# Optimization experiments

Measured on AMD Instinct MI355X. Metric: run time of the kernel, lower is better.

Reference implementation:

```python
import jax, jax.numpy as jnp
import numpy as np

N_RAYS = 65536
S_UNIFORM = 256          # 2 * n_samples coarse samples per ray
N_IMP = 128              # importance samples per ray
TRUNCATION = 2.0 / 512.0 * 4.0  # default in sdf2weights


def raw2weights_occupancy(raw):
    # raw2outputs_nerf_color with occupancy=True
    alpha = jax.nn.sigmoid(10.0 * raw)  # [N, S]
    trans = jnp.cumprod(
        jnp.concatenate([jnp.ones_like(alpha[:, :1]), 1.0 - alpha + 1e-10], axis=-1),
        axis=-1,
    )[:, :-1]
    return alpha, alpha * trans


def sample_pdf_det(bins, weights, n_samples):
    # bins: [N, M], weights: [N, M-1]; deterministic (det=True) inverse-CDF sampling
    w = weights + 1e-5
    pdf = w / jnp.sum(w, axis=-1, keepdims=True)
    cdf = jnp.cumsum(pdf, axis=-1)
    cdf = jnp.concatenate([jnp.zeros_like(cdf[..., :1]), cdf], axis=-1)  # [N, M]
    u = jnp.linspace(0.0, 1.0, n_samples, dtype=cdf.dtype)
    u = jnp.broadcast_to(u, cdf.shape[:-1] + (n_samples,))               # [N, n]
    inds = jax.vmap(lambda c, uu: jnp.searchsorted(c, uu, side='right'))(cdf, u)
    below = jnp.maximum(inds - 1, 0)
    above = jnp.minimum(inds, cdf.shape[-1] - 1)
    cdf_b = jnp.take_along_axis(cdf, below, axis=-1)
    cdf_a = jnp.take_along_axis(cdf, above, axis=-1)
    bins_b = jnp.take_along_axis(bins, below, axis=-1)
    bins_a = jnp.take_along_axis(bins, above, axis=-1)
    denom = cdf_a - cdf_b
    denom = jnp.where(denom < 1e-5, jnp.ones_like(denom), denom)
    t = (u - cdf_b) / denom
    return bins_b + t * (bins_a - bins_b)


def sdf2weights(sdf, z_vals, truncation=TRUNCATION, sc_factor=1.0):
    alpha = jax.nn.sigmoid(sdf / truncation) * jax.nn.sigmoid(-sdf / truncation)
    signs = sdf[:, 1:] * sdf[:, :-1]
    sign_mask = jnp.where(signs < 0.0, 1.0, 0.0)
    inds = jnp.argmax(sign_mask, axis=1)[:, None]              # first zero-crossing
    z_min = jnp.take_along_axis(z_vals, inds, axis=1)          # [N, 1]
    trunc_mask = jnp.where(z_vals < z_min + sc_factor * truncation, 1.0, 0.0)
    alpha = alpha * trunc_mask
    weights = alpha / (jnp.sum(alpha, axis=-1, keepdims=True) + 1e-8)
    return weights


def setup_inputs() -> dict:
    key = jax.random.key(0)
    k1, k2, k3, k4 = jax.random.split(key, 4)
    occ = jax.random.normal(k1, (N_RAYS, S_UNIFORM), dtype=jnp.float32)
    # monotonically increasing depths in [0.1, 4.1)
    z_vals_u = jnp.sort(
        jax.random.uniform(k2, (N_RAYS, S_UNIFORM), dtype=jnp.float32) * 4.0 + 0.1,
        axis=-1,
    )
    sdf = jax.random.normal(k3, (N_RAYS, N_IMP), dtype=jnp.float32) * 0.05
    rgbs = jax.random.uniform(k4, (N_RAYS, N_IMP, 3), dtype=jnp.float32)
    return {"occ": occ, "z_vals_u": z_vals_u, "sdf": sdf, "rgbs": rgbs}


def reference(occ, z_vals_u, sdf, rgbs):
    # 1) coarse occupancy compositing -> weights
    _, w_u = raw2weights_occupancy(occ)
    # 2) inverse-CDF importance sampling over midpoints (detached, as in gen_samples)
    z_mid = 0.5 * (z_vals_u[..., 1:] + z_vals_u[..., :-1])
    z_samples = jax.lax.stop_gradient(sample_pdf_det(z_mid, w_u[..., 1:-1], N_IMP))
    # 3) TSDF weights at importance samples
    weights = sdf2weights(sdf, z_samples)
    # 4) composite
    rgb_map = jnp.clip(jnp.sum(weights[..., None] * rgbs, axis=-2), 0.0, 1.0)  # [N,3]
    depth_map = jnp.sum(weights * z_samples, axis=-1)                          # [N]
    return jnp.concatenate([rgb_map, depth_map[:, None], weights], axis=-1)    # [N, 4+N_IMP]
```

## Files before the change

### kernel.cpp

```cpp
#include <hip/hip_runtime.h>

#define S_U 256
#define N_IMP 128
#define OUT_STRIDE (4 + N_IMP)
#define TRUNC 0.015625f
#define WPB 4
#define INV127 (1.0f / 127.0f)
#define MERGE_N 384

template <int CTRL, int ROWM>
__device__ __forceinline__ float dppf(float identity, float x) {
    return __int_as_float(__builtin_amdgcn_update_dpp(
        __float_as_int(identity), __float_as_int(x), CTRL, ROWM, 0xf, false));
}

__device__ __forceinline__ float wscan_add(float x) {
    x += dppf<0x111, 0xf>(0.f, x);
    x += dppf<0x112, 0xf>(0.f, x);
    x += dppf<0x114, 0xf>(0.f, x);
    x += dppf<0x118, 0xf>(0.f, x);
    x += dppf<0x142, 0xa>(0.f, x);
    x += dppf<0x143, 0xc>(0.f, x);
    return x;
}

__device__ __forceinline__ float wscan_mul(float x) {
    x *= dppf<0x111, 0xf>(1.f, x);
    x *= dppf<0x112, 0xf>(1.f, x);
    x *= dppf<0x114, 0xf>(1.f, x);
    x *= dppf<0x118, 0xf>(1.f, x);
    x *= dppf<0x142, 0xa>(1.f, x);
    x *= dppf<0x143, 0xc>(1.f, x);
    return x;
}

__device__ __forceinline__ int wscan_add_i(int x) {
    x += __builtin_amdgcn_update_dpp(0, x, 0x111, 0xf, 0xf, false);
    x += __builtin_amdgcn_update_dpp(0, x, 0x112, 0xf, 0xf, false);
    x += __builtin_amdgcn_update_dpp(0, x, 0x114, 0xf, 0xf, false);
    x += __builtin_amdgcn_update_dpp(0, x, 0x118, 0xf, 0xf, false);
    x += __builtin_amdgcn_update_dpp(0, x, 0x142, 0xa, 0xf, false);
    x += __builtin_amdgcn_update_dpp(0, x, 0x143, 0xc, 0xf, false);
    return x;
}

__device__ __forceinline__ int wscan_min(int x) {
    const int I = 0x7fffffff;
    x = min(x, __builtin_amdgcn_update_dpp(I, x, 0x111, 0xf, 0xf, false));
    x = min(x, __builtin_amdgcn_update_dpp(I, x, 0x112, 0xf, 0xf, false));
    x = min(x, __builtin_amdgcn_update_dpp(I, x, 0x114, 0xf, 0xf, false));
    x = min(x, __builtin_amdgcn_update_dpp(I, x, 0x118, 0xf, 0xf, false));
    x = min(x, __builtin_amdgcn_update_dpp(I, x, 0x142, 0xa, 0xf, false));
    x = min(x, __builtin_amdgcn_update_dpp(I, x, 0x143, 0xc, 0xf, false));
    return x;
}

__device__ __forceinline__ int k_of(float c) {
    int k = (int)ceilf(c * 127.0f);
    k = min(max(k, 0), 128);
    if (k > 0 && c <= (float)(k - 1) * INV127) --k;
    else if (k < 128 && !(c <= (float)k * INV127)) ++k;
    return k;
}

__global__ __launch_bounds__(256) void tsdf_render_kernel(
    const float* __restrict__ occ,
    const float* __restrict__ zvals,
    const float* __restrict__ sdf,
    const float* __restrict__ rgbs,
    float* __restrict__ out)
{
    const int lane = threadIdx.x & 63;
    const int wv   = threadIdx.x >> 6;
    const int ray  = blockIdx.x * WPB + wv;

    __shared__ __align__(16) float2 s_pair[WPB][S_U];
    __shared__ __align__(16) int s_A[WPB][MERGE_N];
    __shared__ int s_below[WPB][N_IMP];

    const float4 o4 = ((const float4*)(occ   + (size_t)ray * S_U))[lane];
    const float4 z4 = ((const float4*)(zvals + (size_t)ray * S_U))[lane];
    const float2 sd2 = ((const float2*)(sdf + (size_t)ray * N_IMP))[lane];
    const float2* rg = (const float2*)(rgbs + (size_t)ray * (N_IMP * 3)) + lane * 3;
    const float2 p0 = rg[0];
    const float2 p1 = rg[1];
    const float2 p2 = rg[2];

    int4* Az = (int4*)s_A[wv];
    Az[lane] = make_int4(0, 0, 0, 0);
    if (lane < 32) Az[64 + lane] = make_int4(0, 0, 0, 0);

    float a0 = 1.0f / (1.0f + __expf(-10.0f * o4.x));
    float a1 = 1.0f / (1.0f + __expf(-10.0f * o4.y));
    float a2 = 1.0f / (1.0f + __expf(-10.0f * o4.z));
    float a3 = 1.0f / (1.0f + __expf(-10.0f * o4.w));
    float t0 = 1.0f - a0 + 1e-10f;
    float t1 = 1.0f - a1 + 1e-10f;
    float t2 = 1.0f - a2 + 1e-10f;
    float t3 = 1.0f - a3 + 1e-10f;
    float pp0 = t0, pp1 = pp0 * t1, pp2 = pp1 * t2, pp3 = pp2 * t3;
    float ip = wscan_mul(pp3);
    float pbase = __shfl_up(ip, 1);
    if (lane == 0) pbase = 1.0f;

    float w0 = a0 * pbase;
    float w1 = a1 * pbase * pp0;
    float w2 = a2 * pbase * pp1;
    float w3 = a3 * pbase * pp2;

    float v0 = (lane > 0)  ? w0 + 1e-5f : 0.0f;
    float v1 = w1 + 1e-5f;
    float v2 = w2 + 1e-5f;
    float v3 = (lane < 63) ? w3 + 1e-5f : 0.0f;
    float s0 = v0, s1 = s0 + v1, s2 = s1 + v2, s3 = s2 + v3;
    float is = wscan_add(s3);
    float total = __shfl(is, 63);
    float sbase = __shfl_up(is, 1);
    if (lane == 0) sbase = 0.0f;
    float invt = 1.0f / total;

    float c0 = (sbase + s0) * invt;
    float c1 = (sbase + s1) * invt;
    float c2 = (sbase + s2) * invt;
    float c3 = (sbase + s3) * invt;

    float znext = __shfl_down(z4.x, 1);
    float zm0 = 0.5f * (z4.x + z4.y);
    float zm1 = 0.5f * (z4.y + z4.z);
    float zm2 = 0.5f * (z4.z + z4.w);
    float zm3 = 0.5f * (z4.w + znext);

    float2* pr = s_pair[wv];
    *(float4*)&pr[lane * 4 + 0] = make_float4(c0, zm0, c1, zm1);
    *(float4*)&pr[lane * 4 + 2] = make_float4(c2, zm2, c3, zm3);

    int k0 = k_of(c0), k1 = k_of(c1), k2 = k_of(c2), k3 = k_of(c3);
    int base = lane * 4;
    int* Aw = s_A[wv];
    __builtin_amdgcn_wave_barrier();
    Aw[base + 0 + k0] = 1;
    Aw[base + 1 + k1] = 1;
    Aw[base + 2 + k2] = 1;
    if (base + 3 < 255) Aw[base + 3 + k3] = 1;
    __builtin_amdgcn_wave_barrier();

    const int2 r0 = *(const int2*)&Aw[6 * lane + 0];
    const int2 r1 = *(const int2*)&Aw[6 * lane + 2];
    const int2 r2 = *(const int2*)&Aw[6 * lane + 4];
    int q0 = r0.x, q1 = r0.y, q2 = r1.x, q3 = r1.y, q4 = r2.x, q5 = r2.y;
    int e1 = q0, e2 = e1 + q1, e3 = e2 + q2, e4 = e3 + q3, e5 = e4 + q4;
    int tot = e5 + q5;
    int incl = wscan_add_i(tot);
    int sb = __shfl_up(incl, 1);
    if (lane == 0) sb = 0;

    int* bel = s_below[wv];
    int pbase6 = 6 * lane;
    {
        int Sx, j;
        Sx = sb;      j = pbase6 + 0 - Sx; if (!q0 && j < 128) bel[j] = Sx - 1;
        Sx = sb + e1; j = pbase6 + 1 - Sx; if (!q1 && j < 128) bel[j] = Sx - 1;
        Sx = sb + e2; j = pbase6 + 2 - Sx; if (!q2 && j < 128) bel[j] = Sx - 1;
        Sx = sb + e3; j = pbase6 + 3 - Sx; if (!q3 && j < 128) bel[j] = Sx - 1;
        Sx = sb + e4; j = pbase6 + 4 - Sx; if (!q4 && j < 128) bel[j] = Sx - 1;
        Sx = sb + e5; j = pbase6 + 5 - Sx; if (!q5 && j < 128) bel[j] = Sx - 1;
    }
    __builtin_amdgcn_wave_barrier();

    const int2 bb = *(const int2*)&bel[2 * lane];
    int b0 = bb.x, b1 = bb.y;
    float2 pb0 = pr[b0];
    float2 pa0 = pr[min(b0 + 1, 254)];
    float2 pb1 = pr[b1];
    float2 pa1 = pr[min(b1 + 1, 254)];

    float u0 = (float)(2 * lane)     * INV127;
    float u1 = (float)(2 * lane + 1) * INV127;
    float d0 = pa0.x - pb0.x; d0 = (d0 < 1e-5f) ? 1.0f : d0;
    float d1 = pa1.x - pb1.x; d1 = (d1 < 1e-5f) ? 1.0f : d1;
    float zs0 = pb0.y + ((u0 - pb0.x) / d0) * (pa0.y - pb0.y);
    float zs1 = pb1.y + ((u1 - pb1.x) / d1) * (pa1.y - pb1.y);

    float sn = __shfl_down(sd2.x, 1);
    int c = 0x7fffffff;
    if (sd2.x * sd2.y < 0.0f)                 c = 2 * lane;
    else if (lane < 63 && sd2.y * sn < 0.0f)  c = 2 * lane + 1;
    c = wscan_min(c);
    int ci = __shfl(c, 63);
    if (ci == 0x7fffffff) ci = 0;
    float zca = __shfl(zs0, ci >> 1);
    float zcb = __shfl(zs1, ci >> 1);
    float z_min = (ci & 1) ? zcb : zca;

    float x0 = sd2.x * (1.0f / TRUNC);
    float x1 = sd2.y * (1.0f / TRUNC);
    float al0 = 1.0f / (2.0f + __expf(x0) + __expf(-x0));
    float al1 = 1.0f / (2.0f + __expf(x1) + __expf(-x1));
    float zlim = z_min + TRUNC;
    if (!(zs0 < zlim)) al0 = 0.0f;
    if (!(zs1 < zlim)) al1 = 0.0f;

    float sA = wscan_add(al0 + al1);
    float sR = wscan_add(al0 * p0.x + al1 * p1.y);
    float sG = wscan_add(al0 * p0.y + al1 * p2.x);
    float sB = wscan_add(al0 * p1.x + al1 * p2.y);
    float sD = wscan_add(al0 * zs0  + al1 * zs1);

    float asum = __shfl(sA, 63);
    float inv_s = 1.0f / (asum + 1e-8f);

    float* ob = out + (size_t)ray * OUT_STRIDE;
    ((float2*)(ob + 4))[lane] = make_float2(al0 * inv_s, al1 * inv_s);
    if (lane == 63) {
        float inv63 = 1.0f / (sA + 1e-8f);
        ob[0] = fminf(fmaxf(sR * inv63, 0.0f), 1.0f);
        ob[1] = fminf(fmaxf(sG * inv63, 0.0f), 1.0f);
        ob[2] = fminf(fmaxf(sB * inv63, 0.0f), 1.0f);
        ob[3] = sD * inv63;
    }
}

extern "C" void kernel_launch(void* const* d_in, const int* in_sizes, int n_in,
                              void* d_out, int out_size, void* d_ws, size_t ws_size,
                              hipStream_t stream) {
    const float* occ  = (const float*)d_in[0];
    const float* z    = (const float*)d_in[1];
    const float* sdf  = (const float*)d_in[2];
    const float* rgbs = (const float*)d_in[3];
    float* out = (float*)d_out;
    const int n_rays = in_sizes[0] / S_U;
    hipLaunchKernelGGL(tsdf_render_kernel, dim3(n_rays / WPB), dim3(256), 0, stream,
                       occ, z, sdf, rgbs, out);
}
```

Before: 271.1 us.

## Process multiple rays per wave with software-prefetched next-ray loads

Each wave now loops over eight consecutive rays instead of handling one. Inside the loop it issues the next ray's global loads before computing the current ray, so memory latency overlaps with compute. The grid shrinks by a factor of eight, which reduces launch and per-wave setup cost but lowers the number of resident waves available to hide latency. It also raises register pressure from holding the prefetched values.

```diff
diff --git a/kernel.cpp b/kernel.cpp
--- a/kernel.cpp
+++ b/kernel.cpp
@@ -5,6 +5,7 @@
 #define OUT_STRIDE (4 + N_IMP)
 #define TRUNC 0.015625f
 #define WPB 4
+#define RPW 8
 #define INV127 (1.0f / 127.0f)
 #define MERGE_N 384
 
@@ -72,151 +73,167 @@
 {
     const int lane = threadIdx.x & 63;
     const int wv   = threadIdx.x >> 6;
-    const int ray  = blockIdx.x * WPB + wv;
+    const int wave = blockIdx.x * WPB + wv;
+    const int ray0 = wave * RPW;
 
     __shared__ __align__(16) float2 s_pair[WPB][S_U];
     __shared__ __align__(16) int s_A[WPB][MERGE_N];
     __shared__ int s_below[WPB][N_IMP];
 
-    const float4 o4 = ((const float4*)(occ   + (size_t)ray * S_U))[lane];
-    const float4 z4 = ((const float4*)(zvals + (size_t)ray * S_U))[lane];
-    const float2 sd2 = ((const float2*)(sdf + (size_t)ray * N_IMP))[lane];
-    const float2* rg = (const float2*)(rgbs + (size_t)ray * (N_IMP * 3)) + lane * 3;
-    const float2 p0 = rg[0];
-    const float2 p1 = rg[1];
-    const float2 p2 = rg[2];
-
-    int4* Az = (int4*)s_A[wv];
-    Az[lane] = make_int4(0, 0, 0, 0);
-    if (lane < 32) Az[64 + lane] = make_int4(0, 0, 0, 0);
-
-    float a0 = 1.0f / (1.0f + __expf(-10.0f * o4.x));
-    float a1 = 1.0f / (1.0f + __expf(-10.0f * o4.y));
-    float a2 = 1.0f / (1.0f + __expf(-10.0f * o4.z));
-    float a3 = 1.0f / (1.0f + __expf(-10.0f * o4.w));
-    float t0 = 1.0f - a0 + 1e-10f;
-    float t1 = 1.0f - a1 + 1e-10f;
-    float t2 = 1.0f - a2 + 1e-10f;
-    float t3 = 1.0f - a3 + 1e-10f;
-    float pp0 = t0, pp1 = pp0 * t1, pp2 = pp1 * t2, pp3 = pp2 * t3;
-    float ip = wscan_mul(pp3);
-    float pbase = __shfl_up(ip, 1);
-    if (lane == 0) pbase = 1.0f;
-
-    float w0 = a0 * pbase;
-    float w1 = a1 * pbase * pp0;
-    float w2 = a2 * pbase * pp1;
-    float w3 = a3 * pbase * pp2;
-
-    float v0 = (lane > 0)  ? w0 + 1e-5f : 0.0f;
-    float v1 = w1 + 1e-5f;
-    float v2 = w2 + 1e-5f;
-    float v3 = (lane < 63) ? w3 + 1e-5f : 0.0f;
-    float s0 = v0, s1 = s0 + v1, s2 = s1 + v2, s3 = s2 + v3;
-    float is = wscan_add(s3);
-    float total = __shfl(is, 63);
-    float sbase = __shfl_up(is, 1);
-    if (lane == 0) sbase = 0.0f;
-    float invt = 1.0f / total;
-
-    float c0 = (sbase + s0) * invt;
-    float c1 = (sbase + s1) * invt;
-    float c2 = (sbase + s2) * invt;
-    float c3 = (sbase + s3) * invt;
-
-    float znext = __shfl_down(z4.x, 1);
-    float zm0 = 0.5f * (z4.x + z4.y);
-    float zm1 = 0.5f * (z4.y + z4.z);
-    float zm2 = 0.5f * (z4.z + z4.w);
-    float zm3 = 0.5f * (z4.w + znext);
-
-    float2* pr = s_pair[wv];
-    *(float4*)&pr[lane * 4 + 0] = make_float4(c0, zm0, c1, zm1);
-    *(float4*)&pr[lane * 4 + 2] = make_float4(c2, zm2, c3, zm3);
-
-    int k0 = k_of(c0), k1 = k_of(c1), k2 = k_of(c2), k3 = k_of(c3);
-    int base = lane * 4;
-    int* Aw = s_A[wv];
-    __builtin_amdgcn_wave_barrier();
-    Aw[base + 0 + k0] = 1;
-    Aw[base + 1 + k1] = 1;
-    Aw[base + 2 + k2] = 1;
-    if (base + 3 < 255) Aw[base + 3 + k3] = 1;
-    __builtin_amdgcn_wave_barrier();
-
-    const int2 r0 = *(const int2*)&Aw[6 * lane + 0];
-    const int2 r1 = *(const int2*)&Aw[6 * lane + 2];
-    const int2 r2 = *(const int2*)&Aw[6 * lane + 4];
-    int q0 = r0.x, q1 = r0.y, q2 = r1.x, q3 = r1.y, q4 = r2.x, q5 = r2.y;
-    int e1 = q0, e2 = e1 + q1, e3 = e2 + q2, e4 = e3 + q3, e5 = e4 + q4;
-    int tot = e5 + q5;
-    int incl = wscan_add_i(tot);
-    int sb = __shfl_up(incl, 1);
-    if (lane == 0) sb = 0;
-
-    int* bel = s_below[wv];
-    int pbase6 = 6 * lane;
-    {
-        int Sx, j;
-        Sx = sb;      j = pbase6 + 0 - Sx; if (!q0 && j < 128) bel[j] = Sx - 1;
-        Sx = sb + e1; j = pbase6 + 1 - Sx; if (!q1 && j < 128) bel[j] = Sx - 1;
-        Sx = sb + e2; j = pbase6 + 2 - Sx; if (!q2 && j < 128) bel[j] = Sx - 1;
-        Sx = sb + e3; j = pbase6 + 3 - Sx; if (!q3 && j < 128) bel[j] = Sx - 1;
-        Sx = sb + e4; j = pbase6 + 4 - Sx; if (!q4 && j < 128) bel[j] = Sx - 1;
-        Sx = sb + e5; j = pbase6 + 5 - Sx; if (!q5 && j < 128) bel[j] = Sx - 1;
-    }
-    __builtin_amdgcn_wave_barrier();
-
-    const int2 bb = *(const int2*)&bel[2 * lane];
-    int b0 = bb.x, b1 = bb.y;
-    float2 pb0 = pr[b0];
-    float2 pa0 = pr[min(b0 + 1, 254)];
-    float2 pb1 = pr[b1];
-    float2 pa1 = pr[min(b1 + 1, 254)];
-
-    float u0 = (float)(2 * lane)     * INV127;
-    float u1 = (float)(2 * lane + 1) * INV127;
-    float d0 = pa0.x - pb0.x; d0 = (d0 < 1e-5f) ? 1.0f : d0;
-    float d1 = pa1.x - pb1.x; d1 = (d1 < 1e-5f) ? 1.0f : d1;
-    float zs0 = pb0.y + ((u0 - pb0.x) / d0) * (pa0.y - pb0.y);
-    float zs1 = pb1.y + ((u1 - pb1.x) / d1) * (pa1.y - pb1.y);
-
-    float sn = __shfl_down(sd2.x, 1);
-    int c = 0x7fffffff;
-    if (sd2.x * sd2.y < 0.0f)                 c = 2 * lane;
-    else if (lane < 63 && sd2.y * sn < 0.0f)  c = 2 * lane + 1;
-    c = wscan_min(c);
-    int ci = __shfl(c, 63);
-    if (ci == 0x7fffffff) ci = 0;
-    float zca = __shfl(zs0, ci >> 1);
-    float zcb = __shfl(zs1, ci >> 1);
-    float z_min = (ci & 1) ? zcb : zca;
-
-    float x0 = sd2.x * (1.0f / TRUNC);
-    float x1 = sd2.y * (1.0f / TRUNC);
-    float al0 = 1.0f / (2.0f + __expf(x0) + __expf(-x0));
-    float al1 = 1.0f / (2.0f + __expf(x1) + __expf(-x1));
-    float zlim = z_min + TRUNC;
-    if (!(zs0 < zlim)) al0 = 0.0f;
-    if (!(zs1 < zlim)) al1 = 0.0f;
-
-    float sA = wscan_add(al0 + al1);
-    float sR = wscan_add(al0 * p0.x + al1 * p1.y);
-    float sG = wscan_add(al0 * p0.y + al1 * p2.x);
-    float sB = wscan_add(al0 * p1.x + al1 * p2.y);
-    float sD = wscan_add(al0 * zs0  + al1 * zs1);
-
-    float asum = __shfl(sA, 63);
-    float inv_s = 1.0f / (asum + 1e-8f);
-
-    float* ob = out + (size_t)ray * OUT_STRIDE;
-    ((float2*)(ob + 4))[lane] = make_float2(al0 * inv_s, al1 * inv_s);
-    if (lane == 63) {
-        float inv63 = 1.0f / (sA + 1e-8f);
-        ob[0] = fminf(fmaxf(sR * inv63, 0.0f), 1.0f);
-        ob[1] = fminf(fmaxf(sG * inv63, 0.0f), 1.0f);
-        ob[2] = fminf(fmaxf(sB * inv63, 0.0f), 1.0f);
-        ob[3] = sD * inv63;
+    float2* pr  = s_pair[wv];
+    int*    Aw  = s_A[wv];
+    int*    bel = s_below[wv];
+
+    const float4* po = (const float4*)(occ   + (size_t)ray0 * S_U) + lane;
+    const float4* pz = (const float4*)(zvals + (size_t)ray0 * S_U) + lane;
+    const float2* ps = (const float2*)(sdf   + (size_t)ray0 * N_IMP) + lane;
+    const float2* pg = (const float2*)(rgbs  + (size_t)ray0 * (N_IMP * 3)) + lane * 3;
+    float* pout = out + (size_t)ray0 * OUT_STRIDE;
+
+    const float u0 = (float)(2 * lane)     * INV127;
+    const float u1 = (float)(2 * lane + 1) * INV127;
+
+    float4 o4 = *po, z4 = *pz;
+    float2 sd2 = *ps, p0 = pg[0], p1 = pg[1], p2 = pg[2];
+
+#pragma unroll 2
+    for (int r = 0; r < RPW; ++r) {
+        float4 o4n, z4n; float2 sd2n, p0n, p1n, p2n;
+        if (r + 1 < RPW) {
+            po += S_U / 4; pz += S_U / 4; ps += N_IMP / 2; pg += (N_IMP * 3) / 2;
+            o4n = *po; z4n = *pz; sd2n = *ps;
+            p0n = pg[0]; p1n = pg[1]; p2n = pg[2];
+        }
+
+        int4* Az = (int4*)Aw;
+        Az[lane] = make_int4(0, 0, 0, 0);
+        if (lane < 32) Az[64 + lane] = make_int4(0, 0, 0, 0);
+
+        float a0 = 1.0f / (1.0f + __expf(-10.0f * o4.x));
+        float a1 = 1.0f / (1.0f + __expf(-10.0f * o4.y));
+        float a2 = 1.0f / (1.0f + __expf(-10.0f * o4.z));
+        float a3 = 1.0f / (1.0f + __expf(-10.0f * o4.w));
+        float t0 = 1.0f - a0 + 1e-10f;
+        float t1 = 1.0f - a1 + 1e-10f;
+        float t2 = 1.0f - a2 + 1e-10f;
+        float t3 = 1.0f - a3 + 1e-10f;
+        float pp0 = t0, pp1 = pp0 * t1, pp2 = pp1 * t2, pp3 = pp2 * t3;
+        float ip = wscan_mul(pp3);
+        float pbase = __shfl_up(ip, 1);
+        if (lane == 0) pbase = 1.0f;
+
+        float w0 = a0 * pbase;
+        float w1 = a1 * pbase * pp0;
+        float w2 = a2 * pbase * pp1;
+        float w3 = a3 * pbase * pp2;
+
+        float v0 = (lane > 0)  ? w0 + 1e-5f : 0.0f;
+        float v1 = w1 + 1e-5f;
+        float v2 = w2 + 1e-5f;
+        float v3 = (lane < 63) ? w3 + 1e-5f : 0.0f;
+        float s0 = v0, s1 = s0 + v1, s2 = s1 + v2, s3 = s2 + v3;
+        float is = wscan_add(s3);
+        float total = __shfl(is, 63);
+        float sbase = __shfl_up(is, 1);
+        if (lane == 0) sbase = 0.0f;
+        float invt = 1.0f / total;
+
+        float c0 = (sbase + s0) * invt;
+        float c1 = (sbase + s1) * invt;
+        float c2 = (sbase + s2) * invt;
+        float c3 = (sbase + s3) * invt;
+
+        float znext = __shfl_down(z4.x, 1);
+        float zm0 = 0.5f * (z4.x + z4.y);
+        float zm1 = 0.5f * (z4.y + z4.z);
+        float zm2 = 0.5f * (z4.z + z4.w);
+        float zm3 = 0.5f * (z4.w + znext);
+
+        *(float4*)&pr[lane * 4 + 0] = make_float4(c0, zm0, c1, zm1);
+        *(float4*)&pr[lane * 4 + 2] = make_float4(c2, zm2, c3, zm3);
+
+        int k0 = k_of(c0), k1 = k_of(c1), k2 = k_of(c2), k3 = k_of(c3);
+        int base = lane * 4;
+        __builtin_amdgcn_wave_barrier();
+        Aw[base + 0 + k0] = 1;
+        Aw[base + 1 + k1] = 1;
+        Aw[base + 2 + k2] = 1;
+        if (base + 3 < 255) Aw[base + 3 + k3] = 1;
+        __builtin_amdgcn_wave_barrier();
+
+        const int2 r0 = *(const int2*)&Aw[6 * lane + 0];
+        const int2 r1 = *(const int2*)&Aw[6 * lane + 2];
+        const int2 r2 = *(const int2*)&Aw[6 * lane + 4];
+        int q0 = r0.x, q1 = r0.y, q2 = r1.x, q3 = r1.y, q4 = r2.x, q5 = r2.y;
+        int e1 = q0, e2 = e1 + q1, e3 = e2 + q2, e4 = e3 + q3, e5 = e4 + q4;
+        int tot = e5 + q5;
+        int incl = wscan_add_i(tot);
+        int sb = __shfl_up(incl, 1);
+        if (lane == 0) sb = 0;
+
+        int pbase6 = 6 * lane;
+        {
+            int Sx, j;
+            Sx = sb;      j = pbase6 + 0 - Sx; if (!q0 && j < 128) bel[j] = Sx - 1;
+            Sx = sb + e1; j = pbase6 + 1 - Sx; if (!q1 && j < 128) bel[j] = Sx - 1;
+            Sx = sb + e2; j = pbase6 + 2 - Sx; if (!q2 && j < 128) bel[j] = Sx - 1;
+            Sx = sb + e3; j = pbase6 + 3 - Sx; if (!q3 && j < 128) bel[j] = Sx - 1;
+            Sx = sb + e4; j = pbase6 + 4 - Sx; if (!q4 && j < 128) bel[j] = Sx - 1;
+            Sx = sb + e5; j = pbase6 + 5 - Sx; if (!q5 && j < 128) bel[j] = Sx - 1;
+        }
+        __builtin_amdgcn_wave_barrier();
+
+        const int2 bb = *(const int2*)&bel[2 * lane];
+        int b0 = bb.x, b1 = bb.y;
+        float2 pb0 = pr[b0];
+        float2 pa0 = pr[min(b0 + 1, 254)];
+        float2 pb1 = pr[b1];
+        float2 pa1 = pr[min(b1 + 1, 254)];
+
+        float d0 = pa0.x - pb0.x; d0 = (d0 < 1e-5f) ? 1.0f : d0;
+        float d1 = pa1.x - pb1.x; d1 = (d1 < 1e-5f) ? 1.0f : d1;
+        float zs0 = pb0.y + ((u0 - pb0.x) / d0) * (pa0.y - pb0.y);
+        float zs1 = pb1.y + ((u1 - pb1.x) / d1) * (pa1.y - pb1.y);
+
+        float sn = __shfl_down(sd2.x, 1);
+        int c = 0x7fffffff;
+        if (sd2.x * sd2.y < 0.0f)                 c = 2 * lane;
+        else if (lane < 63 && sd2.y * sn < 0.0f)  c = 2 * lane + 1;
+        c = wscan_min(c);
+        int ci = __shfl(c, 63);
+        if (ci == 0x7fffffff) ci = 0;
+        float zca = __shfl(zs0, ci >> 1);
+        float zcb = __shfl(zs1, ci >> 1);
+        float z_min = (ci & 1) ? zcb : zca;
+
+        float x0 = sd2.x * (1.0f / TRUNC);
+        float x1 = sd2.y * (1.0f / TRUNC);
+        float al0 = 1.0f / (2.0f + __expf(x0) + __expf(-x0));
+        float al1 = 1.0f / (2.0f + __expf(x1) + __expf(-x1));
+        float zlim = z_min + TRUNC;
+        if (!(zs0 < zlim)) al0 = 0.0f;
+        if (!(zs1 < zlim)) al1 = 0.0f;
+
+        float sA = wscan_add(al0 + al1);
+        float sR = wscan_add(al0 * p0.x + al1 * p1.y);
+        float sG = wscan_add(al0 * p0.y + al1 * p2.x);
+        float sB = wscan_add(al0 * p1.x + al1 * p2.y);
+        float sD = wscan_add(al0 * zs0  + al1 * zs1);
+
+        float asum = __shfl(sA, 63);
+        float inv_s = 1.0f / (asum + 1e-8f);
+
+        ((float2*)(pout + 4))[lane] = make_float2(al0 * inv_s, al1 * inv_s);
+        if (lane == 63) {
+            float inv63 = 1.0f / (sA + 1e-8f);
+            pout[0] = fminf(fmaxf(sR * inv63, 0.0f), 1.0f);
+            pout[1] = fminf(fmaxf(sG * inv63, 0.0f), 1.0f);
+            pout[2] = fminf(fmaxf(sB * inv63, 0.0f), 1.0f);
+            pout[3] = sD * inv63;
+        }
+        pout += OUT_STRIDE;
+
+        o4 = o4n; z4 = z4n; sd2 = sd2n; p0 = p0n; p1 = p1n; p2 = p2n;
     }
 }
 
@@ -229,6 +246,6 @@
     const float* rgbs = (const float*)d_in[3];
     float* out = (float*)d_out;
     const int n_rays = in_sizes[0] / S_U;
-    hipLaunchKernelGGL(tsdf_render_kernel, dim3(n_rays / WPB), dim3(256), 0, stream,
+    hipLaunchKernelGGL(tsdf_render_kernel, dim3(n_rays / (WPB * RPW)), dim3(256), 0, stream,
                        occ, z, sdf, rgbs, out);
 }
```

Measured after the change: 282.1 us. 1.04x slower.
